# Kernel tuning notes

Hardware: AMD Instinct MI355X
Metric: run time of the kernel (lower is better)

The kernel has to match this reference:

```python
import jax, jax.numpy as jnp
import numpy as np

S, B, D, H, F = 2048, 4, 256, 8, 2048
HD = D // H


def _ln(x, g, b, eps=1e-5):
    mu = jnp.mean(x, axis=-1, keepdims=True)
    var = jnp.var(x, axis=-1, keepdims=True)
    return (x - mu) * jax.lax.rsqrt(var + eps) * g + b


def setup_inputs() -> dict:
    key = jax.random.key(0)
    ks = jax.random.split(key, 8)
    s = lambda fan: 1.0 / np.sqrt(fan)
    return {
        "features": jax.random.normal(ks[0], (S, B, D), jnp.float32),
        "ln_g": jnp.ones((D,), jnp.float32),
        "ln_b": jnp.zeros((D,), jnp.float32),
        "in_proj_w": jax.random.normal(ks[1], (3 * D, D), jnp.float32) * s(D),
        "in_proj_b": jnp.zeros((3 * D,), jnp.float32),
        "out_proj_w": jax.random.normal(ks[2], (D, D), jnp.float32) * s(D),
        "out_proj_b": jnp.zeros((D,), jnp.float32),
        "w1": jax.random.normal(ks[3], (F, D), jnp.float32) * s(D),
        "b1": jnp.zeros((F,), jnp.float32),
        "w2": jax.random.normal(ks[4], (D, F), jnp.float32) * s(F),
        "b2": jnp.zeros((D,), jnp.float32),
    }


def _attn_tanh_relu(x, in_proj_w, in_proj_b, out_proj_w, out_proj_b):
    # x: (S, B, D). Standard MHA projections, but relu(tanh(.)) replaces softmax.
    qkv = x @ in_proj_w.T + in_proj_b            # (S, B, 3D)
    q, k, v = jnp.split(qkv, 3, axis=-1)
    q = q.reshape(S, B, H, HD) * (1.0 / np.sqrt(HD))
    k = k.reshape(S, B, H, HD)
    v = v.reshape(S, B, H, HD)
    scores = jnp.einsum("sbhd,tbhd->bhst", q, k)  # (B, H, S, S)
    w = jax.nn.relu(jnp.tanh(scores))
    out = jnp.einsum("bhst,tbhd->sbhd", w, v).reshape(S, B, D)
    return out @ out_proj_w.T + out_proj_b


def reference(features, ln_g, ln_b, in_proj_w, in_proj_b, out_proj_w, out_proj_b, w1, b1, w2, b2):
    ln_x = _ln(features, ln_g, ln_b)
    attn = _attn_tanh_relu(ln_x, in_proj_w, in_proj_b, out_proj_w, out_proj_b)
    r1 = _ln(ln_x + attn, ln_g, ln_b)
    ff = jax.nn.relu(r1 @ w1.T + b1) @ w2.T + b2
    return _ln(r1 + ff, ln_g, ln_b)
```

## Files before the change

### kernel.cpp

```cpp
#include <hip/hip_runtime.h>
#include <hip/hip_bf16.h>

#define SS 2048
#define BB 4
#define DD 256
#define HH 8
#define HDD 32
#define FFD 2048
#define MM (SS*BB)

typedef __attribute__((ext_vector_type(8))) __bf16 bf16x8;
typedef __attribute__((ext_vector_type(2))) __bf16 bf16x2;
typedef __attribute__((ext_vector_type(8))) short short8;
typedef __attribute__((ext_vector_type(4))) short short4v;
typedef __attribute__((ext_vector_type(4))) float f32x4;
typedef __attribute__((ext_vector_type(16))) float f32x16;
typedef __attribute__((ext_vector_type(2))) unsigned uint2v;
typedef __attribute__((ext_vector_type(4))) unsigned uint4v;

__device__ __forceinline__ unsigned short f2bf(float f) {
  union { float f; unsigned u; } v; v.f = f;
  unsigned r = v.u + 0x7fffu + ((v.u >> 16) & 1u);
  return (unsigned short)(r >> 16);
}

__device__ __forceinline__ float bf2f(short s) {
  union { float f; unsigned u; } v;
  v.u = ((unsigned)(unsigned short)s) << 16;
  return v.f;
}

__device__ __forceinline__ unsigned pk2(float a, float b) {
  bf16x2 t; t[0] = (__bf16)a; t[1] = (__bf16)b;
  return __builtin_bit_cast(unsigned, t);
}

__device__ __forceinline__ void gload16(const void* g, void* l) {
  __builtin_amdgcn_global_load_lds(
      (const __attribute__((address_space(1))) void*)g,
      (__attribute__((address_space(3))) void*)l, 16, 0, 0);
}

__global__ __launch_bounds__(256)
void cvt_ln(const float* __restrict__ a, const float* __restrict__ b,
            const float* __restrict__ c, const float* __restrict__ d,
            short* __restrict__ oa, short* __restrict__ ob,
            short* __restrict__ oc, short* __restrict__ od,
            const float* __restrict__ feat,
            const float* __restrict__ gam, const float* __restrict__ bet,
            float* __restrict__ lnf, short* __restrict__ lnb)
{
  const int y = blockIdx.y;
  if (y < 4) {
    const float* in; short* out; int n4;
    if (y == 0)      { in = a; out = oa; n4 = 768 * 256 / 4; }
    else if (y == 1) { in = b; out = ob; n4 = 256 * 256 / 4; }
    else if (y == 2) { in = c; out = oc; n4 = 2048 * 256 / 4; }
    else             { in = d; out = od; n4 = 2048 * 256 / 4; }
    const int i = blockIdx.x * 256 + threadIdx.x;
    if (i < n4) {
      float4 x = ((const float4*)in)[i];
      short4v o = { (short)f2bf(x.x), (short)f2bf(x.y), (short)f2bf(x.z), (short)f2bf(x.w) };
      ((short4v*)out)[i] = o;
    }
    return;
  }
  const int w = threadIdx.x >> 6, l = threadIdx.x & 63;
  const size_t row = (size_t)blockIdx.x * 4 + w;
  float4 x = *(const float4*)&feat[row * 256 + l * 4];
  float sum = x.x + x.y + x.z + x.w;
  float sq  = x.x*x.x + x.y*x.y + x.z*x.z + x.w*x.w;
#pragma unroll
  for (int off = 32; off > 0; off >>= 1) {
    sum += __shfl_xor(sum, off);
    sq  += __shfl_xor(sq, off);
  }
  const float mu = sum * (1.f / 256.f);
  const float rs = rsqrtf(sq * (1.f / 256.f) - mu * mu + 1e-5f);
  const float4 g4 = *(const float4*)&gam[l * 4];
  const float4 b4 = *(const float4*)&bet[l * 4];
  const float y0 = (x.x - mu) * rs * g4.x + b4.x;
  const float y1 = (x.y - mu) * rs * g4.y + b4.y;
  const float y2 = (x.z - mu) * rs * g4.z + b4.z;
  const float y3 = (x.w - mu) * rs * g4.w + b4.w;
  float4 o; o.x = y0; o.y = y1; o.z = y2; o.w = y3;
  *(float4*)&lnf[row * 256 + l * 4] = o;
  short4v ob2 = { (short)f2bf(y0), (short)f2bf(y1), (short)f2bf(y2), (short)f2bf(y3) };
  *(short4v*)&lnb[row * 256 + l * 4] = ob2;
}

template<int NIN, int WF, int WBF, int BFI>
__global__ __launch_bounds__(256)
void ln_kernel(const float* __restrict__ xa, const void* __restrict__ xb,
               const void* __restrict__ xc,
               const float* __restrict__ gam, const float* __restrict__ bet,
               float* __restrict__ outf, short* __restrict__ outb)
{
  const int w = threadIdx.x >> 6, l = threadIdx.x & 63;
  const size_t row = (size_t)blockIdx.x * 4 + w;
  float4 x = *(const float4*)&xa[row * 256 + l * 4];
  if (NIN >= 2) {
    if (BFI) {
      const short4v yb = *(const short4v*)&((const short*)xb)[row * 256 + l * 4];
      x.x += bf2f(yb[0]); x.y += bf2f(yb[1]); x.z += bf2f(yb[2]); x.w += bf2f(yb[3]);
    } else {
      const float4 yv = *(const float4*)&((const float*)xb)[row * 256 + l * 4];
      x.x += yv.x; x.y += yv.y; x.z += yv.z; x.w += yv.w;
    }
  }
  if (NIN >= 3) {
    if (BFI) {
      const short4v yc = *(const short4v*)&((const short*)xc)[row * 256 + l * 4];
      x.x += bf2f(yc[0]); x.y += bf2f(yc[1]); x.z += bf2f(yc[2]); x.w += bf2f(yc[3]);
    } else {
      const float4 yv = *(const float4*)&((const float*)xc)[row * 256 + l * 4];
      x.x += yv.x; x.y += yv.y; x.z += yv.z; x.w += yv.w;
    }
  }
  float sum = x.x + x.y + x.z + x.w;
  float sq  = x.x*x.x + x.y*x.y + x.z*x.z + x.w*x.w;
#pragma unroll
  for (int off = 32; off > 0; off >>= 1) {
    sum += __shfl_xor(sum, off);
    sq  += __shfl_xor(sq, off);
  }
  const float mu = sum * (1.f / 256.f);
  const float rs = rsqrtf(sq * (1.f / 256.f) - mu * mu + 1e-5f);
  const float4 g4 = *(const float4*)&gam[l * 4];
  const float4 b4 = *(const float4*)&bet[l * 4];
  const float y0 = (x.x - mu) * rs * g4.x + b4.x;
  const float y1 = (x.y - mu) * rs * g4.y + b4.y;
  const float y2 = (x.z - mu) * rs * g4.z + b4.z;
  const float y3 = (x.w - mu) * rs * g4.w + b4.w;
  if (WF) {
    float4 o; o.x = y0; o.y = y1; o.z = y2; o.w = y3;
    *(float4*)&outf[row * 256 + l * 4] = o;
  }
  if (WBF) {
    short4v o = { (short)f2bf(y0), (short)f2bf(y1), (short)f2bf(y2), (short)f2bf(y3) };
    *(short4v*)&outb[row * 256 + l * 4] = o;
  }
}

template<int EPI, int BM, int BN, int KW>
__global__ __launch_bounds__(256)
void gemm_bt(const short* __restrict__ A, const short* __restrict__ W,
             const float* __restrict__ bias, void* __restrict__ out,
             void* __restrict__ out2, int K, int N, int Ksub)
{
  __shared__ short sA[2][BM * 64];
  __shared__ short sB[2][BN * 64];
  const int tid = threadIdx.x;
  const int l  = tid & 63;
  const int w  = tid >> 6;
  const int wr = w >> 1, wc = w & 1;
  const int lr = l & 15, lg = l >> 4;
  const long row0 = (long)blockIdx.y * BM;
  const long col0 = (long)blockIdx.x * BN;
  const int kz = blockIdx.z;
  const int kbeg = kz * Ksub;
  const int ldsw = (tid & ~63) * 16;
  constexpr int MR = BM / 32, NR = BN / 32;
  f32x4 acc[MR][NR] = {};
  const int nt = Ksub / 64;

  auto stage = [&](int buf, int k0) {
#pragma unroll
    for (int i = 0; i < BM / 32; i++) {
      const int o = (i * 256 + tid) * 16;
      const int r = o >> 7;
      const int cg = ((o >> 4) & 7) ^ (r & 7);
      gload16((const char*)A + ((row0 + r) * (long)K + k0) * 2 + cg * 16,
              (char*)sA[buf] + i * 4096 + ldsw);
    }
    const long wstride = KW ? KW : K;
    const long wk = KW ? (k0 & (KW - 1)) : k0;
#pragma unroll
    for (int i = 0; i < BN / 32; i++) {
      const int o = (i * 256 + tid) * 16;
      const int r = o >> 7;
      const int cg = ((o >> 4) & 7) ^ (r & 7);
      gload16((const char*)W + ((col0 + r) * wstride + wk) * 2 + cg * 16,
              (char*)sB[buf] + i * 4096 + ldsw);
    }
  };

  stage(0, kbeg);
  __syncthreads();
  int cur = 0;
  for (int t = 0; t < nt; t++) {
    if (t + 1 < nt) stage(cur ^ 1, kbeg + (t + 1) * 64);
    bf16x8 af[MR][2], bw[NR][2];
#pragma unroll
    for (int m = 0; m < MR; m++)
#pragma unroll
      for (int kk = 0; kk < 2; kk++) {
        const int row = wr * (BM/2) + m * 16 + lr;
        af[m][kk] = *(const bf16x8*)&sA[cur][row * 64 + (((kk*4 + lg) ^ (lr & 7)) * 8)];
      }
#pragma unroll
    for (int n = 0; n < NR; n++)
#pragma unroll
      for (int kk = 0; kk < 2; kk++) {
        const int row = wc * (BN/2) + n * 16 + lr;
        bw[n][kk] = *(const bf16x8*)&sB[cur][row * 64 + (((kk*4 + lg) ^ (lr & 7)) * 8)];
      }
#pragma unroll
    for (int kk = 0; kk < 2; kk++)
#pragma unroll
      for (int m = 0; m < MR; m++)
#pragma unroll
        for (int n = 0; n < NR; n++)
          acc[m][n] = __builtin_amdgcn_mfma_f32_16x16x32_bf16(af[m][kk], bw[n][kk], acc[m][n], 0, 0, 0);
    __syncthreads();
    cur ^= 1;
  }

#pragma unroll
  for (int m = 0; m < MR; m++) {
    const long rbase = row0 + wr * (BM/2) + m * 16 + lg * 4;
#pragma unroll
    for (int n = 0; n < NR; n++) {
      const long c = col0 + wc * (BN/2) + n * 16 + lr;
      const float bv = (EPI == 3 && kz) ? 0.f : bias[c];
#pragma unroll
      for (int j = 0; j < 4; j++) {
        const long r = rbase + j;
        float val = acc[m][n][j] + bv;
        if (EPI == 0) {
          const int part = (int)(c >> 8);
          const int cc = (int)(c & 255);
          const int h = cc >> 5, hd = cc & 31;
          const int bi = (int)(r & 3);
          const int s = (int)(r >> 2);
          const int bh = bi * HH + h;
          if (part == 0) val *= 0.51006972771029396f;
          size_t idx;
          if (part == 2) {
            idx = (size_t)2 * (MM * DD) + (size_t)bh * (SS * HDD)
                + (size_t)(s >> 3) * (HDD * 8) + hd * 8 + (s & 7);
          } else {
            idx = (size_t)part * (MM * DD) + ((size_t)bh * SS + s) * HDD + hd;
          }
          ((short*)out)[idx] = (short)f2bf(val);
        } else if (EPI == 1) {
          ((float*)out)[(size_t)r * N + c] = val;
        } else if (EPI == 2) {
          ((short*)out)[(size_t)r * N + c] = (short)f2bf(fmaxf(val, 0.f));
        } else {
          short* op = kz ? (short*)out2 : (short*)out;
          op[(size_t)r * N + c] = (short)f2bf(val);
        }
      }
    }
  }
}

__global__ __launch_bounds__(256, 4)
void attn_kernel(const short* __restrict__ Qb, const short* __restrict__ Kb,
                 const short* __restrict__ Vb, short* __restrict__ Aout)
{
  const int tid = threadIdx.x;
  const int l = tid & 63, w = tid >> 6;
  const int q32 = l & 31, hf = l >> 5;
  const int i = blockIdx.x;
  const int j = i >> 3;
  const int p = (i & 7) + 8 * (j >> 5);
  const int rem = j & 31;
  const int q0 = (rem >> 1) * 128 + w * 32;
  const int kz = rem & 1;
  const int kbeg = kz * (SS / 2);
  const int kend = kbeg + SS / 2;
  const size_t base = (size_t)p * SS * HDD;
  const short* Q  = Qb + base;
  const short* Kp = Kb + base;
  const short* Vp = Vb + base;

  const short* qrow = &Q[(size_t)(q0 + q32) * HDD];
  const bf16x8 qf0 = *(const bf16x8*)&qrow[hf * 8];
  const bf16x8 qf1 = *(const bf16x8*)&qrow[16 + hf * 8];

  const f32x16 fzero = {};
  f32x16 accA = {}, accB = {};

  auto loadK = [&](int t0, bf16x8* kf) {
    const short* kr = &Kp[(size_t)(t0 + q32) * HDD];
    kf[0] = *(const bf16x8*)&kr[hf * 8];
    kf[1] = *(const bf16x8*)&kr[16 + hf * 8];
  };
  auto loadV = [&](int t0, bf16x8* vf) {
    const short* vb = &Vp[(size_t)((t0 >> 3) + hf) * (HDD * 8) + q32 * 8];
    vf[0] = *(const bf16x8*)&vb[0];
    vf[1] = *(const bf16x8*)&vb[2 * (HDD * 8)];
  };

  auto step = [&](const bf16x8* kf, const bf16x8* vf, f32x16& acc) {
    f32x16 s = __builtin_amdgcn_mfma_f32_32x32x16_bf16(kf[0], qf0, fzero, 0, 0, 0);
    s = __builtin_amdgcn_mfma_f32_32x32x16_bf16(kf[1], qf1, s, 0, 0, 0);
    float pv[16];
#pragma unroll
    for (int r = 0; r < 16; r++) {
      const float e = __builtin_amdgcn_exp2f(s[r]);
      pv[r] = fmaxf(1.f - 2.f * __builtin_amdgcn_rcpf(e + 1.f), 0.f);
    }
    unsigned X0 = pk2(pv[0], pv[1]),   X1 = pk2(pv[2], pv[3]);
    unsigned X2 = pk2(pv[4], pv[5]),   X3 = pk2(pv[6], pv[7]);
    unsigned X4 = pk2(pv[8], pv[9]),   X5 = pk2(pv[10], pv[11]);
    unsigned X6 = pk2(pv[12], pv[13]), X7 = pk2(pv[14], pv[15]);
    uint2v r02 = __builtin_amdgcn_permlane32_swap(X0, X2, false, false);
    uint2v r13 = __builtin_amdgcn_permlane32_swap(X1, X3, false, false);
    uint2v r46 = __builtin_amdgcn_permlane32_swap(X4, X6, false, false);
    uint2v r57 = __builtin_amdgcn_permlane32_swap(X5, X7, false, false);
    const uint4v f0 = { r02[0], r13[0], r02[1], r13[1] };
    const uint4v f1 = { r46[0], r57[0], r46[1], r57[1] };
    const bf16x8 pa0 = __builtin_bit_cast(bf16x8, f0);
    const bf16x8 pa1 = __builtin_bit_cast(bf16x8, f1);
    acc = __builtin_amdgcn_mfma_f32_32x32x16_bf16(pa0, vf[0], acc, 0, 0, 0);
    acc = __builtin_amdgcn_mfma_f32_32x32x16_bf16(pa1, vf[1], acc, 0, 0, 0);
  };

  bf16x8 kA[2], vA[2], kB[2], vB[2];
  loadK(kbeg, kA); loadV(kbeg, vA);
  for (int t0 = kbeg; t0 < kend; t0 += 64) {
    loadK(t0 + 32, kB); loadV(t0 + 32, vB);
    step(kA, vA, accA);
    const int tn = (t0 + 64 < kend) ? t0 + 64 : kbeg;
    loadK(tn, kA); loadV(tn, vA);
    step(kB, vB, accB);
  }

  const int bi = p >> 3, hh = p & 7;
  const size_t colo = (size_t)kz * DD + (size_t)hh * HDD + q32;
#pragma unroll
  for (int r = 0; r < 16; r++) {
    const int crow = (r & 3) + 8 * (r >> 2) + 4 * hf;
    Aout[((size_t)(q0 + crow) * BB + bi) * (2 * DD) + colo] =
        (short)f2bf(accA[r] + accB[r]);
  }
}

extern "C" void kernel_launch(void* const* d_in, const int* in_sizes, int n_in,
                              void* d_out, int out_size, void* d_ws, size_t ws_size,
                              hipStream_t stream) {
  const float* features   = (const float*)d_in[0];
  const float* ln_g       = (const float*)d_in[1];
  const float* ln_b       = (const float*)d_in[2];
  const float* in_proj_w  = (const float*)d_in[3];
  const float* in_proj_b  = (const float*)d_in[4];
  const float* out_proj_w = (const float*)d_in[5];
  const float* out_proj_b = (const float*)d_in[6];
  const float* w1 = (const float*)d_in[7];
  const float* b1 = (const float*)d_in[8];
  const float* w2 = (const float*)d_in[9];
  const float* b2 = (const float*)d_in[10];

  char* ws = (char*)d_ws;
  const size_t MB = 1024 * 1024;
  float* lnx_f  = (float*)(ws + 0);
  short* lnx_b  = (short*)(ws + 8 * MB);
  short* qkv    = (short*)(ws + 12 * MB);
  short* aprt   = (short*)(ws + 24 * MB);
  float* proj   = (float*)(ws + 12 * MB);
  short* r1_b   = (short*)(ws + 20 * MB);
  float* r1_f   = (float*)(ws + 24 * MB);
  short* h1     = (short*)(ws + 32 * MB);
  short* ffb    = (short*)(ws + 12 * MB);
  short* ffp1   = (short*)(ws + 16 * MB);
  short* wqkv_b = (short*)(ws + 64 * MB);
  short* wout_b = wqkv_b + 768 * 256;
  short* w1_b   = wout_b + 256 * 256;
  short* w2_b   = w1_b + 2048 * 256;

  cvt_ln<<<dim3(2048, 5), 256, 0, stream>>>(in_proj_w, out_proj_w, w1, w2,
                                            wqkv_b, wout_b, w1_b, w2_b,
                                            features, ln_g, ln_b, lnx_f, lnx_b);

  gemm_bt<0, 128, 64, 0><<<dim3(12, 64, 1), 256, 0, stream>>>(lnx_b, wqkv_b, in_proj_b, qkv, nullptr, 256, 768, 256);

  attn_kernel<<<dim3(1024, 1, 1), 256, 0, stream>>>(qkv, qkv + 2097152, qkv + 2 * 2097152, aprt);

  gemm_bt<1, 64, 64, 256><<<dim3(4, 128, 1), 256, 0, stream>>>(aprt, wout_b, out_proj_b, proj, nullptr, 512, 256, 512);

  ln_kernel<2, 1, 1, 0><<<2048, 256, 0, stream>>>(lnx_f, proj, nullptr, ln_g, ln_b, r1_f, r1_b);

  gemm_bt<2, 128, 128, 0><<<dim3(16, 64, 1), 256, 0, stream>>>(r1_b, w1_b, b1, h1, nullptr, 256, 2048, 256);

  gemm_bt<3, 128, 64, 0><<<dim3(4, 64, 2), 256, 0, stream>>>(h1, w2_b, b2, ffb, ffp1, 2048, 256, 1024);

  ln_kernel<3, 1, 0, 1><<<2048, 256, 0, stream>>>(r1_f, ffb, ffp1, ln_g, ln_b, (float*)d_out, nullptr);
}
```

Before: 124.7 us.

## Drop attention key-split, use 512-thread blocks, emit bf16 out-proj and compact conversion grid

Attention no longer splits the key range into two halves whose partial outputs are concatenated. Each 512-thread block (8 waves) now processes 256 queries over the full key sequence, which halves the attention output width and the out-proj GEMM K dimension. The out-proj GEMM writes bf16 through a new epilogue, and the following LayerNorm reads bf16 instead of fp32. Weight conversion is packed into a single grid row so no blocks sit idle, at the cost of fewer attention blocks and longer serial loops per wave.

After: 124.7 us. About the same (+0.0%).

```diff
diff --git a/kernel.cpp b/kernel.cpp
--- a/kernel.cpp
+++ b/kernel.cpp
@@ -50,19 +50,17 @@
             const float* __restrict__ gam, const float* __restrict__ bet,
             float* __restrict__ lnf, short* __restrict__ lnb)
 {
-  const int y = blockIdx.y;
-  if (y < 4) {
-    const float* in; short* out; int n4;
-    if (y == 0)      { in = a; out = oa; n4 = 768 * 256 / 4; }
-    else if (y == 1) { in = b; out = ob; n4 = 256 * 256 / 4; }
-    else if (y == 2) { in = c; out = oc; n4 = 2048 * 256 / 4; }
-    else             { in = d; out = od; n4 = 2048 * 256 / 4; }
-    const int i = blockIdx.x * 256 + threadIdx.x;
-    if (i < n4) {
-      float4 x = ((const float4*)in)[i];
-      short4v o = { (short)f2bf(x.x), (short)f2bf(x.y), (short)f2bf(x.z), (short)f2bf(x.w) };
-      ((short4v*)out)[i] = o;
-    }
+  if (blockIdx.y == 1) {
+    const int bx = blockIdx.x;
+    if (bx >= 1280) return;
+    const float* in; short* out; int i;
+    if (bx < 192)      { in = a; out = oa; i = bx * 256 + threadIdx.x; }
+    else if (bx < 256) { in = b; out = ob; i = (bx - 192) * 256 + threadIdx.x; }
+    else if (bx < 768) { in = c; out = oc; i = (bx - 256) * 256 + threadIdx.x; }
+    else               { in = d; out = od; i = (bx - 768) * 256 + threadIdx.x; }
+    float4 x = ((const float4*)in)[i];
+    short4v o = { (short)f2bf(x.x), (short)f2bf(x.y), (short)f2bf(x.z), (short)f2bf(x.w) };
+    ((short4v*)out)[i] = o;
     return;
   }
   const int w = threadIdx.x >> 6, l = threadIdx.x & 63;
@@ -243,20 +241,20 @@
             idx = (size_t)part * (MM * DD) + ((size_t)bh * SS + s) * HDD + hd;
           }
           ((short*)out)[idx] = (short)f2bf(val);
-        } else if (EPI == 1) {
-          ((float*)out)[(size_t)r * N + c] = val;
         } else if (EPI == 2) {
           ((short*)out)[(size_t)r * N + c] = (short)f2bf(fmaxf(val, 0.f));
-        } else {
+        } else if (EPI == 3) {
           short* op = kz ? (short*)out2 : (short*)out;
           op[(size_t)r * N + c] = (short)f2bf(val);
+        } else {
+          ((short*)out)[(size_t)r * N + c] = (short)f2bf(val);
         }
       }
     }
   }
 }
 
-__global__ __launch_bounds__(256, 4)
+__global__ __launch_bounds__(512, 4)
 void attn_kernel(const short* __restrict__ Qb, const short* __restrict__ Kb,
                  const short* __restrict__ Vb, short* __restrict__ Aout)
 {
@@ -265,12 +263,8 @@
   const int q32 = l & 31, hf = l >> 5;
   const int i = blockIdx.x;
   const int j = i >> 3;
-  const int p = (i & 7) + 8 * (j >> 5);
-  const int rem = j & 31;
-  const int q0 = (rem >> 1) * 128 + w * 32;
-  const int kz = rem & 1;
-  const int kbeg = kz * (SS / 2);
-  const int kend = kbeg + SS / 2;
+  const int p = (i & 7) + 8 * (j >> 3);
+  const int q0 = (j & 7) * 256 + w * 32;
   const size_t base = (size_t)p * SS * HDD;
   const short* Q  = Qb + base;
   const short* Kp = Kb + base;
@@ -320,21 +314,21 @@
   };
 
   bf16x8 kA[2], vA[2], kB[2], vB[2];
-  loadK(kbeg, kA); loadV(kbeg, vA);
-  for (int t0 = kbeg; t0 < kend; t0 += 64) {
+  loadK(0, kA); loadV(0, vA);
+  for (int t0 = 0; t0 < SS; t0 += 64) {
     loadK(t0 + 32, kB); loadV(t0 + 32, vB);
     step(kA, vA, accA);
-    const int tn = (t0 + 64 < kend) ? t0 + 64 : kbeg;
+    const int tn = (t0 + 64 < SS) ? t0 + 64 : 0;
     loadK(tn, kA); loadV(tn, vA);
     step(kB, vB, accB);
   }
 
   const int bi = p >> 3, hh = p & 7;
-  const size_t colo = (size_t)kz * DD + (size_t)hh * HDD + q32;
+  const size_t colo = (size_t)hh * HDD + q32;
 #pragma unroll
   for (int r = 0; r < 16; r++) {
     const int crow = (r & 3) + 8 * (r >> 2) + 4 * hf;
-    Aout[((size_t)(q0 + crow) * BB + bi) * (2 * DD) + colo] =
+    Aout[((size_t)(q0 + crow) * BB + bi) * DD + colo] =
         (short)f2bf(accA[r] + accB[r]);
   }
 }
@@ -360,7 +354,7 @@
   short* lnx_b  = (short*)(ws + 8 * MB);
   short* qkv    = (short*)(ws + 12 * MB);
   short* aprt   = (short*)(ws + 24 * MB);
-  float* proj   = (float*)(ws + 12 * MB);
+  short* proj   = (short*)(ws + 12 * MB);
   short* r1_b   = (short*)(ws + 20 * MB);
   float* r1_f   = (float*)(ws + 24 * MB);
   short* h1     = (short*)(ws + 32 * MB);
@@ -371,17 +365,17 @@
   short* w1_b   = wout_b + 256 * 256;
   short* w2_b   = w1_b + 2048 * 256;
 
-  cvt_ln<<<dim3(2048, 5), 256, 0, stream>>>(in_proj_w, out_proj_w, w1, w2,
+  cvt_ln<<<dim3(2048, 2), 256, 0, stream>>>(in_proj_w, out_proj_w, w1, w2,
                                             wqkv_b, wout_b, w1_b, w2_b,
                                             features, ln_g, ln_b, lnx_f, lnx_b);
 
   gemm_bt<0, 128, 64, 0><<<dim3(12, 64, 1), 256, 0, stream>>>(lnx_b, wqkv_b, in_proj_b, qkv, nullptr, 256, 768, 256);
 
-  attn_kernel<<<dim3(1024, 1, 1), 256, 0, stream>>>(qkv, qkv + 2097152, qkv + 2 * 2097152, aprt);
-
-  gemm_bt<1, 64, 64, 256><<<dim3(4, 128, 1), 256, 0, stream>>>(aprt, wout_b, out_proj_b, proj, nullptr, 512, 256, 512);
-
-  ln_kernel<2, 1, 1, 0><<<2048, 256, 0, stream>>>(lnx_f, proj, nullptr, ln_g, ln_b, r1_f, r1_b);
+  attn_kernel<<<dim3(256, 1, 1), 512, 0, stream>>>(qkv, qkv + 2097152, qkv + 2 * 2097152, aprt);
+
+  gemm_bt<4, 64, 64, 0><<<dim3(4, 128, 1), 256, 0, stream>>>(aprt, wout_b, out_proj_b, proj, nullptr, 256, 256, 256);
+
+  ln_kernel<2, 1, 1, 1><<<2048, 256, 0, stream>>>(lnx_f, proj, nullptr, ln_g, ln_b, r1_f, r1_b);
 
   gemm_bt<2, 128, 128, 0><<<dim3(16, 64, 1), 256, 0, stream>>>(r1_b, w1_b, b1, h1, nullptr, 256, 2048, 256);
 
```

## Software-pipeline QK^T MFMA ahead of activation in attention loop

Applied to the files above, without the earlier changes.

Restructures the attention inner loop so that the QK^T MFMA for the next 32-key tile is issued before the tanh/relu activation and PV MFMA of the current tile. K loads move one tile further ahead. The goal is to overlap MFMA latency with the transcendental ALU work. This needs more live registers, so the occupancy hint of 4 in launch_bounds is dropped, which may cost occupancy.

After: 127.0 us. No clear change (+1.9%).

```diff
diff --git a/kernel.cpp b/kernel.cpp
--- a/kernel.cpp
+++ b/kernel.cpp
@@ -256,7 +256,7 @@
   }
 }
 
-__global__ __launch_bounds__(256, 4)
+__global__ __launch_bounds__(256)
 void attn_kernel(const short* __restrict__ Qb, const short* __restrict__ Kb,
                  const short* __restrict__ Vb, short* __restrict__ Aout)
 {
@@ -283,20 +283,21 @@
   const f32x16 fzero = {};
   f32x16 accA = {}, accB = {};
 
-  auto loadK = [&](int t0, bf16x8* kf) {
+  auto loadKr = [&](int t0, bf16x8& f0, bf16x8& f1) {
     const short* kr = &Kp[(size_t)(t0 + q32) * HDD];
-    kf[0] = *(const bf16x8*)&kr[hf * 8];
-    kf[1] = *(const bf16x8*)&kr[16 + hf * 8];
+    f0 = *(const bf16x8*)&kr[hf * 8];
+    f1 = *(const bf16x8*)&kr[16 + hf * 8];
   };
-  auto loadV = [&](int t0, bf16x8* vf) {
+  auto loadVr = [&](int t0, bf16x8& f0, bf16x8& f1) {
     const short* vb = &Vp[(size_t)((t0 >> 3) + hf) * (HDD * 8) + q32 * 8];
-    vf[0] = *(const bf16x8*)&vb[0];
-    vf[1] = *(const bf16x8*)&vb[2 * (HDD * 8)];
+    f0 = *(const bf16x8*)&vb[0];
+    f1 = *(const bf16x8*)&vb[2 * (HDD * 8)];
   };
-
-  auto step = [&](const bf16x8* kf, const bf16x8* vf, f32x16& acc) {
-    f32x16 s = __builtin_amdgcn_mfma_f32_32x32x16_bf16(kf[0], qf0, fzero, 0, 0, 0);
-    s = __builtin_amdgcn_mfma_f32_32x32x16_bf16(kf[1], qf1, s, 0, 0, 0);
+  auto qkt = [&](const bf16x8& k0, const bf16x8& k1) -> f32x16 {
+    f32x16 s = __builtin_amdgcn_mfma_f32_32x32x16_bf16(k0, qf0, fzero, 0, 0, 0);
+    return __builtin_amdgcn_mfma_f32_32x32x16_bf16(k1, qf1, s, 0, 0, 0);
+  };
+  auto actpv = [&](const f32x16& s, const bf16x8& v0, const bf16x8& v1, f32x16& acc) {
     float pv[16];
 #pragma unroll
     for (int r = 0; r < 16; r++) {
@@ -315,18 +316,28 @@
     const uint4v f1 = { r46[0], r57[0], r46[1], r57[1] };
     const bf16x8 pa0 = __builtin_bit_cast(bf16x8, f0);
     const bf16x8 pa1 = __builtin_bit_cast(bf16x8, f1);
-    acc = __builtin_amdgcn_mfma_f32_32x32x16_bf16(pa0, vf[0], acc, 0, 0, 0);
-    acc = __builtin_amdgcn_mfma_f32_32x32x16_bf16(pa1, vf[1], acc, 0, 0, 0);
+    acc = __builtin_amdgcn_mfma_f32_32x32x16_bf16(pa0, v0, acc, 0, 0, 0);
+    acc = __builtin_amdgcn_mfma_f32_32x32x16_bf16(pa1, v1, acc, 0, 0, 0);
   };
 
-  bf16x8 kA[2], vA[2], kB[2], vB[2];
-  loadK(kbeg, kA); loadV(kbeg, vA);
+  bf16x8 kA0, kA1, kB0, kB1, vA0, vA1, vB0, vB1;
+  f32x16 sA, sB;
+  loadKr(kbeg, kA0, kA1);
+  loadKr(kbeg + 32, kB0, kB1);
+  loadVr(kbeg, vA0, vA1);
+  sA = qkt(kA0, kA1);
+
   for (int t0 = kbeg; t0 < kend; t0 += 64) {
-    loadK(t0 + 32, kB); loadV(t0 + 32, vB);
-    step(kA, vA, accA);
-    const int tn = (t0 + 64 < kend) ? t0 + 64 : kbeg;
-    loadK(tn, kA); loadV(tn, vA);
-    step(kB, vB, accB);
+    const int tA = (t0 + 64 < kend) ? t0 + 64 : kbeg;
+    loadKr(tA, kA0, kA1);
+    loadVr(t0 + 32, vB0, vB1);
+    sB = qkt(kB0, kB1);
+    actpv(sA, vA0, vA1, accA);
+    const int tB = (t0 + 96 < kend) ? t0 + 96 : kbeg;
+    loadKr(tB, kB0, kB1);
+    loadVr(tA, vA0, vA1);
+    sA = qkt(kA0, kA1);
+    actpv(sB, vB0, vB1, accB);
   }
 
   const int bi = p >> 3, hh = p & 7;
```
